# Kernel optimization log

Hardware: AMD Instinct MI355X
Metric: run time of the kernel (lower is better)

The kernel has to match this reference:

```python
import jax, jax.numpy as jnp
import numpy as np

DIM0, DIMO, WIDTH, DEPTH = 64, 16, 128, 6  # depth = number of weight matrices
N = 524288


def setup_inputs() -> dict:
    key = jax.random.key(0)
    ks = jax.random.split(key, DEPTH + 1)
    x = jax.random.normal(ks[0], (N, DIM0), dtype=jnp.float32)
    bd0 = 1.0 / np.sqrt(DIM0)   # first layer init bound (per torch code)
    bd = 1.0 / np.sqrt(WIDTH)   # remaining layers init bound
    W0 = jax.random.uniform(ks[1], (DIM0, WIDTH), minval=-bd0, maxval=bd0, dtype=jnp.float32)
    W1 = jax.random.uniform(ks[2], (WIDTH, WIDTH), minval=-bd, maxval=bd, dtype=jnp.float32)
    W2 = jax.random.uniform(ks[3], (WIDTH, WIDTH), minval=-bd, maxval=bd, dtype=jnp.float32)
    W3 = jax.random.uniform(ks[4], (WIDTH, WIDTH), minval=-bd, maxval=bd, dtype=jnp.float32)
    W4 = jax.random.uniform(ks[5], (WIDTH, WIDTH), minval=-bd, maxval=bd, dtype=jnp.float32)
    W5 = jax.random.uniform(ks[6], (WIDTH, DIMO), minval=-bd, maxval=bd, dtype=jnp.float32)
    bias = jnp.zeros((DIMO,), dtype=jnp.float32)
    return {"x": x, "W0": W0, "W1": W1, "W2": W2, "W3": W3, "W4": W4, "W5": W5, "bias": bias}


def reference(x, W0, W1, W2, W3, W4, W5, bias):
    # Fully-fused MLP math: matmul (no bias) + ReLU for every layer except the
    # last (output_activation='None'); then cast back to x dtype and add bias.
    h = jax.nn.relu(x @ W0)
    h = jax.nn.relu(h @ W1)
    h = jax.nn.relu(h @ W2)
    h = jax.nn.relu(h @ W3)
    h = jax.nn.relu(h @ W4)
    out = (h @ W5).astype(x.dtype) + bias
    return out
```

## Files before the change

### kernel.cpp

```cpp
#include <hip/hip_runtime.h>
#include <stdint.h>


typedef __bf16 bf16x8 __attribute__((ext_vector_type(8)));
typedef __bf16 bf16x4 __attribute__((ext_vector_type(4)));
typedef float  floatx4 __attribute__((ext_vector_type(4)));

constexpr int NS   = 524288;
constexpr int TILE = 128;
constexpr int NBLK = NS / TILE;

constexpr int WTOT = 9472;

__global__ void prep_weights(const float* __restrict__ W0, const float* __restrict__ W1,
                             const float* __restrict__ W2, const float* __restrict__ W3,
                             const float* __restrict__ W4, const float* __restrict__ W5,
                             bf16x8* __restrict__ ws) {
  int gid = blockIdx.x * blockDim.x + threadIdx.x;
  if (gid >= WTOT) return;
  const float* Wsrc; int nout, KT, base;
  if (gid < 1024)      { Wsrc = W0; nout = 128; KT = 2; base = 0;    }
  else if (gid < 3072) { Wsrc = W1; nout = 128; KT = 4; base = 1024; }
  else if (gid < 5120) { Wsrc = W2; nout = 128; KT = 4; base = 3072; }
  else if (gid < 7168) { Wsrc = W3; nout = 128; KT = 4; base = 5120; }
  else if (gid < 9216) { Wsrc = W4; nout = 128; KT = 4; base = 7168; }
  else                 { Wsrc = W5; nout = 16;  KT = 4; base = 9216; }
  int id  = gid - base;
  int p   = id & 63;
  int l15 = p & 15;
  int g   = p >> 4;
  int blk = id >> 6;
  int kt  = blk % KT;
  int it  = blk / KT;
  int row = it * 16 + l15;
  int kc  = kt * 4 + g;
  bf16x8 v;
#pragma unroll
  for (int j = 0; j < 8; ++j)
    v[j] = (__bf16)Wsrc[(8 * kc + j) * nout + row];
  ws[gid] = v;
}

__device__ __forceinline__ void zero_acc(floatx4 acc[8][2]) {
  floatx4 z = {0.f, 0.f, 0.f, 0.f};
#pragma unroll
  for (int i = 0; i < 8; ++i) {
    acc[i][0] = z; acc[i][1] = z;
  }
}

template <int KT>
__device__ __forceinline__ void layer_mm(const bf16x8* __restrict__ wg,
                                         const bf16x8* Hb, floatx4 acc[8][2],
                                         int n_base, int l15, int g, int lane) {
#pragma unroll
  for (int kt = 0; kt < KT; ++kt) {
    const int cx = (kt * 4 + g) ^ (l15 & 7);
    bf16x8 a[8], b[2];
#pragma unroll
    for (int i = 0; i < 8; ++i) a[i] = wg[((i * KT + kt) << 6) + lane];
    b[0] = Hb[(n_base + l15) * 16 + cx];
    b[1] = Hb[(n_base + 16 + l15) * 16 + cx];
#pragma unroll
    for (int ot = 0; ot < 8; ++ot)
#pragma unroll
      for (int nt = 0; nt < 2; ++nt)
        acc[ot][nt] = __builtin_amdgcn_mfma_f32_16x16x32_bf16(a[ot], b[nt], acc[ot][nt], 0, 0, 0);
  }
}

__device__ __forceinline__ void write_h(bf16x4* H8, const floatx4 acc[8][2],
                                        int n_base, int l15, int g) {
#pragma unroll
  for (int ot = 0; ot < 8; ++ot) {
    int ob    = 16 * ot + 4 * g;
    int phys8 = (((ob >> 3) ^ (l15 & 7)) << 1) | ((ob >> 2) & 1);
#pragma unroll
    for (int nt = 0; nt < 2; ++nt) {
      int s = n_base + 16 * nt + l15;
      floatx4 v = acc[ot][nt];
      bf16x4 h;
      h[0] = (__bf16)fmaxf(v[0], 0.0f);
      h[1] = (__bf16)fmaxf(v[1], 0.0f);
      h[2] = (__bf16)fmaxf(v[2], 0.0f);
      h[3] = (__bf16)fmaxf(v[3], 0.0f);
      H8[s * 32 + phys8] = h;
    }
  }
}

__global__ void __launch_bounds__(256, 3) mlp_kernel(const float* __restrict__ x,
                                                     const float* __restrict__ bias,
                                                     const bf16x8* __restrict__ wimg,
                                                     float* __restrict__ out) {
  __shared__ bf16x8 Hbuf[TILE * 16];

  const int t    = threadIdx.x;
  const int lane = t & 63;
  const int w    = t >> 6;
  const int l15  = lane & 15;
  const int g    = lane >> 4;
  const int n_base = w * 32;
  const int tile = blockIdx.x;

  const float* xt = x + (size_t)tile * TILE * 64 + (size_t)n_base * 64;
#pragma unroll
  for (int i = 0; i < 4; ++i) {
    int f2 = lane + 64 * i;
    int s = f2 >> 3, c = f2 & 7;
    const floatx4* src = (const floatx4*)(xt + f2 * 8);
    floatx4 lo = src[0], hi = src[1];
    bf16x8 v;
    v[0] = (__bf16)lo[0]; v[1] = (__bf16)lo[1]; v[2] = (__bf16)lo[2]; v[3] = (__bf16)lo[3];
    v[4] = (__bf16)hi[0]; v[5] = (__bf16)hi[1]; v[6] = (__bf16)hi[2]; v[7] = (__bf16)hi[3];
    Hbuf[(n_base + s) * 16 + (c ^ (s & 7))] = v;
  }

  floatx4 acc[8][2];

  zero_acc(acc);
  layer_mm<2>(wimg, Hbuf, acc, n_base, l15, g, lane);
  write_h((bf16x4*)Hbuf, acc, n_base, l15, g);

  constexpr int WOFF[5] = {1024, 3072, 5120, 7168, 9216};
#pragma unroll
  for (int l = 0; l < 4; ++l) {
    zero_acc(acc);
    layer_mm<4>(wimg + WOFF[l], Hbuf, acc, n_base, l15, g, lane);
    write_h((bf16x4*)Hbuf, acc, n_base, l15, g);
  }

  floatx4 a5[2];
  {
    floatx4 z = {0.f, 0.f, 0.f, 0.f};
    a5[0] = z; a5[1] = z;
  }
#pragma unroll
  for (int kt = 0; kt < 4; ++kt) {
    int cx = (kt * 4 + g) ^ (l15 & 7);
    bf16x8 a = wimg[9216 + (kt << 6) + lane];
#pragma unroll
    for (int nt = 0; nt < 2; ++nt) {
      bf16x8 b = Hbuf[(n_base + 16 * nt + l15) * 16 + cx];
      a5[nt] = __builtin_amdgcn_mfma_f32_16x16x32_bf16(a, b, a5[nt], 0, 0, 0);
    }
  }
  floatx4 bv = *(const floatx4*)(bias + 4 * g);
  floatx4* outv = (floatx4*)out;
#pragma unroll
  for (int nt = 0; nt < 2; ++nt) {
    int s = tile * TILE + n_base + 16 * nt + l15;
    outv[s * 4 + g] = a5[nt] + bv;
  }
}

extern "C" void kernel_launch(void* const* d_in, const int* in_sizes, int n_in,
                              void* d_out, int out_size, void* d_ws, size_t ws_size,
                              hipStream_t stream) {
  (void)in_sizes; (void)n_in; (void)out_size; (void)ws_size;
  const float* x    = (const float*)d_in[0];
  const float* W0   = (const float*)d_in[1];
  const float* W1   = (const float*)d_in[2];
  const float* W2   = (const float*)d_in[3];
  const float* W3   = (const float*)d_in[4];
  const float* W4   = (const float*)d_in[5];
  const float* W5   = (const float*)d_in[6];
  const float* bias = (const float*)d_in[7];
  bf16x8* ws = (bf16x8*)d_ws;

  prep_weights<<<(WTOT + 255) / 256, 256, 0, stream>>>(W0, W1, W2, W3, W4, W5, ws);
  mlp_kernel<<<NBLK, 256, 0, stream>>>(x, bias, (const bf16x8*)ws, (float*)d_out);
}
```

Measured before the change: 280.4 us.

## Switch to 32x32x16 MFMA with 64 samples per wave and prefetch

Replaces the 16x16x32 bf16 MFMA tiling with 32x32x16 MFMAs. Each wave now owns 64 samples in a private LDS region, and the block tile grows to 256 samples. The weight image is re-laid out for the new A-operand fragment format, with W5 padded to a 32-row tile. Operands for the next k-step are register-prefetched to overlap loads with MFMA. The larger per-wave accumulator (128 floats) raises register pressure, so launch bounds drop from 3 to 2 blocks per SM. The padded last layer does twice the MFMA work it needs.

```diff
diff --git a/kernel.cpp b/kernel.cpp
--- a/kernel.cpp
+++ b/kernel.cpp
@@ -4,13 +4,16 @@
 
 typedef __bf16 bf16x8 __attribute__((ext_vector_type(8)));
 typedef __bf16 bf16x4 __attribute__((ext_vector_type(4)));
-typedef float  floatx4 __attribute__((ext_vector_type(4)));
+typedef float  floatx4  __attribute__((ext_vector_type(4)));
+typedef float  floatx16 __attribute__((ext_vector_type(16)));
 
 constexpr int NS   = 524288;
-constexpr int TILE = 128;
+constexpr int SPW  = 64;
+constexpr int WPB  = 4;
+constexpr int TILE = SPW * WPB;
 constexpr int NBLK = NS / TILE;
 
-constexpr int WTOT = 9472;
+constexpr int WTOT = 9728;
 
 __global__ void prep_weights(const float* __restrict__ W0, const float* __restrict__ W1,
                              const float* __restrict__ W2, const float* __restrict__ W3,
@@ -18,139 +21,164 @@
                              bf16x8* __restrict__ ws) {
   int gid = blockIdx.x * blockDim.x + threadIdx.x;
   if (gid >= WTOT) return;
-  const float* Wsrc; int nout, KT, base;
-  if (gid < 1024)      { Wsrc = W0; nout = 128; KT = 2; base = 0;    }
-  else if (gid < 3072) { Wsrc = W1; nout = 128; KT = 4; base = 1024; }
-  else if (gid < 5120) { Wsrc = W2; nout = 128; KT = 4; base = 3072; }
-  else if (gid < 7168) { Wsrc = W3; nout = 128; KT = 4; base = 5120; }
-  else if (gid < 9216) { Wsrc = W4; nout = 128; KT = 4; base = 7168; }
-  else                 { Wsrc = W5; nout = 16;  KT = 4; base = 9216; }
+  const float* Wsrc; int nout, MT, base;
+  if (gid < 1024)      { Wsrc = W0; nout = 128; MT = 4; base = 0;    }
+  else if (gid < 3072) { Wsrc = W1; nout = 128; MT = 4; base = 1024; }
+  else if (gid < 5120) { Wsrc = W2; nout = 128; MT = 4; base = 3072; }
+  else if (gid < 7168) { Wsrc = W3; nout = 128; MT = 4; base = 5120; }
+  else if (gid < 9216) { Wsrc = W4; nout = 128; MT = 4; base = 7168; }
+  else                 { Wsrc = W5; nout = 16;  MT = 1; base = 9216; }
   int id  = gid - base;
-  int p   = id & 63;
-  int l15 = p & 15;
-  int g   = p >> 4;
-  int blk = id >> 6;
-  int kt  = blk % KT;
-  int it  = blk / KT;
-  int row = it * 16 + l15;
-  int kc  = kt * 4 + g;
+  int l   = id & 63, blk = id >> 6;
+  int mt  = blk % MT, ks = blk / MT;
+  int row = mt * 32 + (l & 31);
+  int k0  = ks * 16 + (l >> 5) * 8;
   bf16x8 v;
 #pragma unroll
   for (int j = 0; j < 8; ++j)
-    v[j] = (__bf16)Wsrc[(8 * kc + j) * nout + row];
+    v[j] = (row < nout) ? (__bf16)Wsrc[(k0 + j) * nout + row] : (__bf16)0.0f;
   ws[gid] = v;
 }
 
-__device__ __forceinline__ void zero_acc(floatx4 acc[8][2]) {
-  floatx4 z = {0.f, 0.f, 0.f, 0.f};
-#pragma unroll
-  for (int i = 0; i < 8; ++i) {
-    acc[i][0] = z; acc[i][1] = z;
-  }
-}
-
-template <int KT>
+__device__ __forceinline__ bf16x8 h_read(const bf16x8* Hw, int nt, int ks, int n31, int h) {
+  int c = 2 * ks + h;
+  int row = nt * 32 + n31;
+  return Hw[row * 16 + (c ^ (n31 & 7))];
+}
+
+template <int KS>
 __device__ __forceinline__ void layer_mm(const bf16x8* __restrict__ wg,
-                                         const bf16x8* Hb, floatx4 acc[8][2],
-                                         int n_base, int l15, int g, int lane) {
-#pragma unroll
-  for (int kt = 0; kt < KT; ++kt) {
-    const int cx = (kt * 4 + g) ^ (l15 & 7);
-    bf16x8 a[8], b[2];
-#pragma unroll
-    for (int i = 0; i < 8; ++i) a[i] = wg[((i * KT + kt) << 6) + lane];
-    b[0] = Hb[(n_base + l15) * 16 + cx];
-    b[1] = Hb[(n_base + 16 + l15) * 16 + cx];
-#pragma unroll
-    for (int ot = 0; ot < 8; ++ot)
-#pragma unroll
-      for (int nt = 0; nt < 2; ++nt)
-        acc[ot][nt] = __builtin_amdgcn_mfma_f32_16x16x32_bf16(a[ot], b[nt], acc[ot][nt], 0, 0, 0);
-  }
-}
-
-__device__ __forceinline__ void write_h(bf16x4* H8, const floatx4 acc[8][2],
-                                        int n_base, int l15, int g) {
-#pragma unroll
-  for (int ot = 0; ot < 8; ++ot) {
-    int ob    = 16 * ot + 4 * g;
-    int phys8 = (((ob >> 3) ^ (l15 & 7)) << 1) | ((ob >> 2) & 1);
-#pragma unroll
-    for (int nt = 0; nt < 2; ++nt) {
-      int s = n_base + 16 * nt + l15;
-      floatx4 v = acc[ot][nt];
-      bf16x4 h;
-      h[0] = (__bf16)fmaxf(v[0], 0.0f);
-      h[1] = (__bf16)fmaxf(v[1], 0.0f);
-      h[2] = (__bf16)fmaxf(v[2], 0.0f);
-      h[3] = (__bf16)fmaxf(v[3], 0.0f);
-      H8[s * 32 + phys8] = h;
+                                         const bf16x8* Hw, floatx16 acc[2][4],
+                                         int l, int n31, int h) {
+  bf16x8 a_cur[4], b_cur[2];
+#pragma unroll
+  for (int mt = 0; mt < 4; ++mt) a_cur[mt] = wg[mt * 64 + l];
+  b_cur[0] = h_read(Hw, 0, 0, n31, h);
+  b_cur[1] = h_read(Hw, 1, 0, n31, h);
+#pragma unroll
+  for (int ks = 0; ks < KS; ++ks) {
+    bf16x8 a_nxt[4], b_nxt[2];
+    if (ks + 1 < KS) {
+#pragma unroll
+      for (int mt = 0; mt < 4; ++mt) a_nxt[mt] = wg[((ks + 1) * 4 + mt) * 64 + l];
+      b_nxt[0] = h_read(Hw, 0, ks + 1, n31, h);
+      b_nxt[1] = h_read(Hw, 1, ks + 1, n31, h);
     }
-  }
-}
-
-__global__ void __launch_bounds__(256, 3) mlp_kernel(const float* __restrict__ x,
+#pragma unroll
+    for (int nt = 0; nt < 2; ++nt)
+#pragma unroll
+      for (int mt = 0; mt < 4; ++mt)
+        acc[nt][mt] = __builtin_amdgcn_mfma_f32_32x32x16_bf16(a_cur[mt], b_cur[nt], acc[nt][mt], 0, 0, 0);
+    if (ks + 1 < KS) {
+#pragma unroll
+      for (int mt = 0; mt < 4; ++mt) a_cur[mt] = a_nxt[mt];
+      b_cur[0] = b_nxt[0]; b_cur[1] = b_nxt[1];
+    }
+  }
+}
+
+__device__ __forceinline__ void zero_acc(floatx16 acc[2][4]) {
+#pragma unroll
+  for (int nt = 0; nt < 2; ++nt)
+#pragma unroll
+    for (int mt = 0; mt < 4; ++mt)
+#pragma unroll
+      for (int r = 0; r < 16; ++r) acc[nt][mt][r] = 0.0f;
+}
+
+__device__ __forceinline__ void write_h(bf16x4* H8, const floatx16 acc[2][4],
+                                        int n31, int h) {
+#pragma unroll
+  for (int nt = 0; nt < 2; ++nt) {
+    int row_s = nt * 32 + n31;
+#pragma unroll
+    for (int mt = 0; mt < 4; ++mt)
+#pragma unroll
+      for (int q = 0; q < 4; ++q) {
+        bf16x4 v;
+#pragma unroll
+        for (int j = 0; j < 4; ++j) v[j] = (__bf16)fmaxf(acc[nt][mt][4 * q + j], 0.0f);
+        int c = 4 * mt + q;
+        H8[row_s * 32 + (c ^ (n31 & 7)) * 2 + h] = v;
+      }
+  }
+}
+
+__global__ void __launch_bounds__(256, 2) mlp_kernel(const float* __restrict__ x,
                                                      const float* __restrict__ bias,
                                                      const bf16x8* __restrict__ wimg,
                                                      float* __restrict__ out) {
-  __shared__ bf16x8 Hbuf[TILE * 16];
-
-  const int t    = threadIdx.x;
-  const int lane = t & 63;
-  const int w    = t >> 6;
-  const int l15  = lane & 15;
-  const int g    = lane >> 4;
-  const int n_base = w * 32;
-  const int tile = blockIdx.x;
-
-  const float* xt = x + (size_t)tile * TILE * 64 + (size_t)n_base * 64;
-#pragma unroll
-  for (int i = 0; i < 4; ++i) {
-    int f2 = lane + 64 * i;
-    int s = f2 >> 3, c = f2 & 7;
-    const floatx4* src = (const floatx4*)(xt + f2 * 8);
-    floatx4 lo = src[0], hi = src[1];
+  __shared__ bf16x8 Hbuf[WPB * 64 * 16];
+
+  const int t   = threadIdx.x;
+  const int l   = t & 63;
+  const int w   = t >> 6;
+  const int n31 = l & 31;
+  const int h   = l >> 5;
+  bf16x8* Hw = Hbuf + w * (64 * 16);
+  const size_t S0 = (size_t)blockIdx.x * TILE + (size_t)w * SPW;
+
+  const float* xw = x + S0 * 64;
+#pragma unroll
+  for (int it = 0; it < 8; ++it) {
+    int id = it * 64 + l, s = id >> 3, c = id & 7;
+    const floatx4* p = (const floatx4*)(xw + id * 8);
+    floatx4 lo = p[0], hi = p[1];
     bf16x8 v;
     v[0] = (__bf16)lo[0]; v[1] = (__bf16)lo[1]; v[2] = (__bf16)lo[2]; v[3] = (__bf16)lo[3];
     v[4] = (__bf16)hi[0]; v[5] = (__bf16)hi[1]; v[6] = (__bf16)hi[2]; v[7] = (__bf16)hi[3];
-    Hbuf[(n_base + s) * 16 + (c ^ (s & 7))] = v;
-  }
-
-  floatx4 acc[8][2];
+    Hw[s * 16 + (c ^ (s & 7))] = v;
+  }
+
+  floatx16 acc[2][4];
 
   zero_acc(acc);
-  layer_mm<2>(wimg, Hbuf, acc, n_base, l15, g, lane);
-  write_h((bf16x4*)Hbuf, acc, n_base, l15, g);
-
-  constexpr int WOFF[5] = {1024, 3072, 5120, 7168, 9216};
-#pragma unroll
-  for (int l = 0; l < 4; ++l) {
+  layer_mm<4>(wimg, Hw, acc, l, n31, h);
+  write_h((bf16x4*)Hw, acc, n31, h);
+
+  constexpr int WOFF[4] = {1024, 3072, 5120, 7168};
+#pragma unroll
+  for (int ly = 0; ly < 4; ++ly) {
     zero_acc(acc);
-    layer_mm<4>(wimg + WOFF[l], Hbuf, acc, n_base, l15, g, lane);
-    write_h((bf16x4*)Hbuf, acc, n_base, l15, g);
-  }
-
-  floatx4 a5[2];
+    layer_mm<8>(wimg + WOFF[ly], Hw, acc, l, n31, h);
+    write_h((bf16x4*)Hw, acc, n31, h);
+  }
+
+  floatx16 a5[2];
+#pragma unroll
+  for (int nt = 0; nt < 2; ++nt)
+#pragma unroll
+    for (int r = 0; r < 16; ++r) a5[nt][r] = 0.0f;
+
   {
-    floatx4 z = {0.f, 0.f, 0.f, 0.f};
-    a5[0] = z; a5[1] = z;
-  }
-#pragma unroll
-  for (int kt = 0; kt < 4; ++kt) {
-    int cx = (kt * 4 + g) ^ (l15 & 7);
-    bf16x8 a = wimg[9216 + (kt << 6) + lane];
-#pragma unroll
-    for (int nt = 0; nt < 2; ++nt) {
-      bf16x8 b = Hbuf[(n_base + 16 * nt + l15) * 16 + cx];
-      a5[nt] = __builtin_amdgcn_mfma_f32_16x16x32_bf16(a, b, a5[nt], 0, 0, 0);
+    const bf16x8* wg5 = wimg + 9216;
+    bf16x8 a_cur = wg5[l];
+    bf16x8 b_cur[2] = {h_read(Hw, 0, 0, n31, h), h_read(Hw, 1, 0, n31, h)};
+#pragma unroll
+    for (int ks = 0; ks < 8; ++ks) {
+      bf16x8 a_nxt; bf16x8 b_nxt[2];
+      if (ks + 1 < 8) {
+        a_nxt = wg5[(ks + 1) * 64 + l];
+        b_nxt[0] = h_read(Hw, 0, ks + 1, n31, h);
+        b_nxt[1] = h_read(Hw, 1, ks + 1, n31, h);
+      }
+      a5[0] = __builtin_amdgcn_mfma_f32_32x32x16_bf16(a_cur, b_cur[0], a5[0], 0, 0, 0);
+      a5[1] = __builtin_amdgcn_mfma_f32_32x32x16_bf16(a_cur, b_cur[1], a5[1], 0, 0, 0);
+      if (ks + 1 < 8) { a_cur = a_nxt; b_cur[0] = b_nxt[0]; b_cur[1] = b_nxt[1]; }
     }
   }
-  floatx4 bv = *(const floatx4*)(bias + 4 * g);
+
+  floatx4 bv0 = *(const floatx4*)(bias + 4 * h);
+  floatx4 bv1 = *(const floatx4*)(bias + 8 + 4 * h);
   floatx4* outv = (floatx4*)out;
 #pragma unroll
   for (int nt = 0; nt < 2; ++nt) {
-    int s = tile * TILE + n_base + 16 * nt + l15;
-    outv[s * 4 + g] = a5[nt] + bv;
+    size_t s = S0 + nt * 32 + n31;
+    floatx4 o0, o1;
+#pragma unroll
+    for (int j = 0; j < 4; ++j) { o0[j] = a5[nt][j] + bv0[j]; o1[j] = a5[nt][4 + j] + bv1[j]; }
+    outv[s * 4 + h]     = o0;
+    outv[s * 4 + 2 + h] = o1;
   }
 }
 
```

Result: no change. 280.1 us (-0.1%).
